# Performance work log

Measured on AMD Instinct MI355X. Metric: run time of the kernel, lower is better.

## Reference

```python
import jax, jax.numpy as jnp
import numpy as np

D = 1024          # label_size / in_features
V = 100000        # vocab size
SHORTLIST = 10000 # cutoffs[0]
# tail clusters: (proj_dim, cluster_size) per div_value=2 schedule
TAILS = [(512, 10000), (256, 20000), (128, 40000), (64, 20000)]


def setup_inputs() -> dict:
    key = jax.random.key(0)
    ks = jax.random.split(key, 11)
    s = jnp.float32(0.02)
    inp = {
        "feature": jax.random.normal(ks[0], (D,), jnp.float32),
        "targets": jax.random.randint(ks[1], (4096,), 0, V),
        "head_w": jax.random.normal(ks[2], (SHORTLIST + len(TAILS), D), jnp.float32) * s,
    }
    for i, (h, c) in enumerate(TAILS):
        inp[f"t{i}p"] = jax.random.normal(ks[3 + 2 * i], (h, D), jnp.float32) * s
        inp[f"t{i}w"] = jax.random.normal(ks[4 + 2 * i], (c, h), jnp.float32) * s
    return inp


def reference(feature, targets, head_w, t0p, t0w, t1p, t1w, t2p, t2w, t3p, t3w):
    # head logits: [SHORTLIST + n_clusters]
    head_lp = jax.nn.log_softmax(head_w @ feature)
    parts = [head_lp[:SHORTLIST]]
    tails = [(t0p, t0w), (t1p, t1w), (t2p, t2w), (t3p, t3w)]
    for i, (p, w) in enumerate(tails):
        # two-stage low-rank projection: [h] then cluster logits [c]
        cl_lp = jax.nn.log_softmax(w @ (p @ feature)) + head_lp[SHORTLIST + i]
        parts.append(cl_lp)
    logprob = jnp.concatenate(parts)  # [V] full-vocab log-probabilities
    return -jnp.mean(logprob[targets])
```

## Files before the change

### kernel.cpp

```cpp
#include <hip/hip_runtime.h>
#include <math.h>

#define NHEAD     10004
#define OFF_HEAD  0
#define OFF_H0    10004
#define OFF_H1    10516
#define OFF_H2    10772
#define OFF_H3    10900
#define OFF_C0    10964
#define OFF_C1    20964
#define OFF_C2    40964
#define OFF_C3    80964
#define OFF_P     100964
#define OFF_PH    100964
#define OFF_P0    101277
#define OFF_P1    101590
#define OFF_P2    101903
#define OFF_P3    102528
#define NPART     1877

__device__ __forceinline__ float wave_sum(float v) {
  v += __shfl_xor(v, 32, 64);
  v += __shfl_xor(v, 16, 64);
  v += __shfl_xor(v, 8, 64);
  v += __shfl_xor(v, 4, 64);
  v += __shfl_xor(v, 2, 64);
  v += __shfl_xor(v, 1, 64);
  return v;
}

__device__ __forceinline__ float dot4(float4 a, float4 c) {
  return a.x * c.x + a.y * c.y + a.z * c.z + a.w * c.w;
}

__global__ __launch_bounds__(256) void proj_kernel(
    const float* __restrict__ feat,
    const float* __restrict__ p0, const float* __restrict__ p1,
    const float* __restrict__ p2, const float* __restrict__ p3,
    float* __restrict__ ws) {
  __shared__ __align__(16) float sf[1024];
  ((float4*)sf)[threadIdx.x] = ((const float4*)feat)[threadIdx.x];
  __syncthreads();
  const float4* sf4 = (const float4*)sf;
  const int wave = threadIdx.x >> 6, lane = threadIdx.x & 63;
  const int pb = blockIdx.x;
#pragma unroll
  for (int k = 0; k < 4; ++k) {
    int row = NHEAD + pb * 16 + wave * 4 + k;
    const float* src;
    if (row < 10516)      src = p0 + (size_t)(row - 10004) * 1024;
    else if (row < 10772) src = p1 + (size_t)(row - 10516) * 1024;
    else if (row < 10900) src = p2 + (size_t)(row - 10772) * 1024;
    else                  src = p3 + (size_t)(row - 10900) * 1024;
    const float4* src4 = (const float4*)src;
    float acc = 0.f;
#pragma unroll
    for (int j = 0; j < 4; ++j) acc += dot4(src4[lane + j * 64], sf4[lane + j * 64]);
    acc = wave_sum(acc);
    if (lane == 0) ws[row] = acc;
  }
}

__global__ __launch_bounds__(256) void main_kernel(
    const float* __restrict__ feat, const float* __restrict__ head_w,
    const float* __restrict__ w0, const float* __restrict__ w1,
    const float* __restrict__ w2, const float* __restrict__ w3,
    float* __restrict__ ws) {
  __shared__ __align__(16) float sh[1024];
  __shared__ float wred[4];
  const int b = blockIdx.x;
  const int wave = threadIdx.x >> 6, lane = threadIdx.x & 63;
  float esum = 0.f;
  int poff, lb;

  if (b < 313) {
    lb = b; poff = OFF_PH;
    ((float4*)sh)[threadIdx.x] = ((const float4*)feat)[threadIdx.x];
    __syncthreads();
    const float4* sf4 = (const float4*)sh;
    const int row0 = lb * 32 + wave * 8;
#pragma unroll
    for (int k = 0; k < 8; ++k) {
      int row = row0 + k;
      int rc = min(row, NHEAD - 1);
      const float4* src4 = (const float4*)head_w + (size_t)rc * 256;
      float acc = 0.f;
#pragma unroll
      for (int j = 0; j < 4; ++j) acc += dot4(src4[lane + j * 64], sf4[lane + j * 64]);
      acc = wave_sum(acc);
      if (lane == 0 && row < NHEAD) { ws[OFF_HEAD + row] = acc; esum += expf(acc); }
    }
  } else if (b < 626) {
    lb = b - 313; poff = OFF_P0;
    if (threadIdx.x < 128) ((float4*)sh)[threadIdx.x] = ((const float4*)(ws + OFF_H0))[threadIdx.x];
    __syncthreads();
    const float4* sh4 = (const float4*)sh;
    const float4 cv0 = sh4[lane], cv1 = sh4[lane + 64];
    const int row0 = lb * 32 + wave * 8;
#pragma unroll
    for (int k = 0; k < 8; ++k) {
      int rc = min(row0 + k, 9999);
      const float4* wr4 = (const float4*)(w0 + (size_t)rc * 512);
      float acc = dot4(wr4[lane], cv0) + dot4(wr4[lane + 64], cv1);
      acc = wave_sum(acc);
      if (lane == 0 && row0 + k < 10000) { ws[OFF_C0 + row0 + k] = acc; esum += expf(acc); }
    }
  } else if (b < 939) {
    lb = b - 626; poff = OFF_P1;
    if (threadIdx.x < 64) ((float4*)sh)[threadIdx.x] = ((const float4*)(ws + OFF_H1))[threadIdx.x];
    __syncthreads();
    const float4 cv = ((const float4*)sh)[lane];
    const int row0 = lb * 64 + wave * 16;
#pragma unroll
    for (int k = 0; k < 16; ++k) {
      int rc = min(row0 + k, 19999);
      float acc = dot4(((const float4*)(w1 + (size_t)rc * 256))[lane], cv);
      acc = wave_sum(acc);
      if (lane == 0 && row0 + k < 20000) { ws[OFF_C1 + row0 + k] = acc; esum += expf(acc); }
    }
  } else if (b < 1564) {
    lb = b - 939; poff = OFF_P2;
    if (threadIdx.x < 32) ((float4*)sh)[threadIdx.x] = ((const float4*)(ws + OFF_H2))[threadIdx.x];
    __syncthreads();
    const float4 cv = ((const float4*)sh)[lane & 31];
    const int row0 = lb * 64 + wave * 16;
#pragma unroll
    for (int p = 0; p < 8; ++p) {
      int rbase = row0 + 2 * p;
      float acc = dot4(((const float4*)w2)[(size_t)rbase * 32 + lane], cv);
      acc += __shfl_xor(acc, 1, 64);
      acc += __shfl_xor(acc, 2, 64);
      acc += __shfl_xor(acc, 4, 64);
      acc += __shfl_xor(acc, 8, 64);
      acc += __shfl_xor(acc, 16, 64);
      if ((lane & 31) == 0) {
        int r = rbase + (lane >> 5);
        ws[OFF_C2 + r] = acc; esum += expf(acc);
      }
    }
  } else {
    lb = b - 1564; poff = OFF_P3;
    if (threadIdx.x < 16) ((float4*)sh)[threadIdx.x] = ((const float4*)(ws + OFF_H3))[threadIdx.x];
    __syncthreads();
    const float4 cv = ((const float4*)sh)[lane & 15];
    const int row0 = lb * 64 + wave * 16;
#pragma unroll
    for (int q = 0; q < 4; ++q) {
      int rb = row0 + 4 * q;
      int rbc = min(rb, 19996);
      float acc = dot4(((const float4*)w3)[(size_t)rbc * 16 + lane], cv);
      acc += __shfl_xor(acc, 1, 64);
      acc += __shfl_xor(acc, 2, 64);
      acc += __shfl_xor(acc, 4, 64);
      acc += __shfl_xor(acc, 8, 64);
      if ((lane & 15) == 0 && rb < 20000) {
        int r = rb + (lane >> 4);
        ws[OFF_C3 + r] = acc; esum += expf(acc);
      }
    }
  }
  esum = wave_sum(esum);
  if (lane == 0) wred[wave] = esum;
  __syncthreads();
  if (threadIdx.x == 0) ws[poff + lb] = wred[0] + wred[1] + wred[2] + wred[3];
}

__global__ __launch_bounds__(1024) void finalize_kernel(
    const int* __restrict__ targets, float* __restrict__ ws,
    float* __restrict__ out) {
  const int wv = threadIdx.x >> 6, lane = threadIdx.x & 63;
  float a0 = 0.f, a1 = 0.f, a2 = 0.f, a3 = 0.f, a4 = 0.f;
#pragma unroll
  for (int it = 0; it < 2; ++it) {
    int i = threadIdx.x + it * 1024;
    if (i < NPART) {
      float v = ws[OFF_P + i];
      if (i < 313)       a0 += v;
      else if (i < 626)  a1 += v;
      else if (i < 939)  a2 += v;
      else if (i < 1564) a3 += v;
      else               a4 += v;
    }
  }
  a0 = wave_sum(a0); a1 = wave_sum(a1); a2 = wave_sum(a2);
  a3 = wave_sum(a3); a4 = wave_sum(a4);
  __shared__ float r5[16][5];
  __shared__ float slse[5];
  if (lane == 0) { r5[wv][0] = a0; r5[wv][1] = a1; r5[wv][2] = a2; r5[wv][3] = a3; r5[wv][4] = a4; }
  __syncthreads();
  if (threadIdx.x < 5) {
    float s = 0.f;
#pragma unroll
    for (int w = 0; w < 16; ++w) s += r5[w][threadIdx.x];
    slse[threadIdx.x] = logf(s);
  }
  __syncthreads();
  const float lse0 = slse[0], lse1 = slse[1], lse2 = slse[2], lse3 = slse[3], lse4 = slse[4];
  const float g0 = ws[10000] - lse0, g1 = ws[10001] - lse0;
  const float g2 = ws[10002] - lse0, g3 = ws[10003] - lse0;
  float s = 0.f;
#pragma unroll
  for (int it = 0; it < 4; ++it) {
    int t = targets[threadIdx.x + it * 1024];
    float lp;
    if (t < 10000)      lp = ws[OFF_HEAD + t] - lse0;
    else if (t < 20000) lp = ws[OFF_C0 + t - 10000] - lse1 + g0;
    else if (t < 40000) lp = ws[OFF_C1 + t - 20000] - lse2 + g1;
    else if (t < 80000) lp = ws[OFF_C2 + t - 40000] - lse3 + g2;
    else                lp = ws[OFF_C3 + t - 80000] - lse4 + g3;
    s += lp;
  }
  s = wave_sum(s);
  if (lane == 0) r5[wv][0] = s;
  __syncthreads();
  if (threadIdx.x == 0) {
    float tot = 0.f;
#pragma unroll
    for (int w = 0; w < 16; ++w) tot += r5[w][0];
    out[0] = -tot * (1.f / 4096.f);
  }
}

extern "C" void kernel_launch(void* const* d_in, const int* in_sizes, int n_in,
                              void* d_out, int out_size, void* d_ws, size_t ws_size,
                              hipStream_t stream) {
  const float* feat    = (const float*)d_in[0];
  const int*   targets = (const int*)d_in[1];
  const float* head_w  = (const float*)d_in[2];
  const float* t0p = (const float*)d_in[3];
  const float* t0w = (const float*)d_in[4];
  const float* t1p = (const float*)d_in[5];
  const float* t1w = (const float*)d_in[6];
  const float* t2p = (const float*)d_in[7];
  const float* t2w = (const float*)d_in[8];
  const float* t3p = (const float*)d_in[9];
  const float* t3w = (const float*)d_in[10];
  float* ws  = (float*)d_ws;
  float* out = (float*)d_out;

  proj_kernel<<<60, 256, 0, stream>>>(feat, t0p, t1p, t2p, t3p, ws);
  main_kernel<<<1877, 256, 0, stream>>>(feat, head_w, t0w, t1w, t2w, t3w, ws);
  finalize_kernel<<<1, 1024, 0, stream>>>(targets, ws, out);
}
```

Measured before the change: 165.8 us.

## Restructure GEMV into per-wave persistent work units with batched loads

The projection kernel now gives one row per wave across 240 blocks, and loads are issued before the dot products. The main kernel becomes a grid-stride loop over per-wave units that cover every section. Each unit first issues 16 float4 loads, then computes and reduces, so more memory requests are in flight per wave. The block-level reduction and syncthreads are dropped in favour of per-wave partial sums. The finalize kernel prefetches target values with branchless addressing, which adds more partials to reduce and more register pressure per unit.

```diff
diff --git a/kernel.cpp b/kernel.cpp
--- a/kernel.cpp
+++ b/kernel.cpp
@@ -4,20 +4,19 @@
 #define NHEAD     10004
 #define OFF_HEAD  0
 #define OFF_H0    10004
-#define OFF_H1    10516
-#define OFF_H2    10772
-#define OFF_H3    10900
 #define OFF_C0    10964
 #define OFF_C1    20964
 #define OFF_C2    40964
 #define OFF_C3    80964
 #define OFF_P     100964
-#define OFF_PH    100964
-#define OFF_P0    101277
-#define OFF_P1    101590
-#define OFF_P2    101903
-#define OFF_P3    102528
-#define NPART     1877
+
+#define U_HEAD 2501
+#define B_C0   2501
+#define B_C1   3751
+#define B_C2   5001
+#define B_C3   6251
+#define NUNITS 6564
+#define NWAVES 3284
 
 __device__ __forceinline__ float wave_sum(float v) {
   v += __shfl_xor(v, 32, 64);
@@ -42,23 +41,133 @@
   ((float4*)sf)[threadIdx.x] = ((const float4*)feat)[threadIdx.x];
   __syncthreads();
   const float4* sf4 = (const float4*)sf;
-  const int wave = threadIdx.x >> 6, lane = threadIdx.x & 63;
-  const int pb = blockIdx.x;
-#pragma unroll
-  for (int k = 0; k < 4; ++k) {
-    int row = NHEAD + pb * 16 + wave * 4 + k;
-    const float* src;
-    if (row < 10516)      src = p0 + (size_t)(row - 10004) * 1024;
-    else if (row < 10772) src = p1 + (size_t)(row - 10516) * 1024;
-    else if (row < 10900) src = p2 + (size_t)(row - 10772) * 1024;
-    else                  src = p3 + (size_t)(row - 10900) * 1024;
-    const float4* src4 = (const float4*)src;
-    float acc = 0.f;
-#pragma unroll
-    for (int j = 0; j < 4; ++j) acc += dot4(src4[lane + j * 64], sf4[lane + j * 64]);
-    acc = wave_sum(acc);
-    if (lane == 0) ws[row] = acc;
-  }
+  const int lane = threadIdx.x & 63;
+  const int pr = blockIdx.x * 4 + (threadIdx.x >> 6);
+  const float* src;
+  if (pr < 512)      src = p0 + (size_t)pr * 1024;
+  else if (pr < 768) src = p1 + (size_t)(pr - 512) * 1024;
+  else if (pr < 896) src = p2 + (size_t)(pr - 768) * 1024;
+  else               src = p3 + (size_t)(pr - 896) * 1024;
+  const float4* src4 = (const float4*)src;
+  float4 ld[4];
+#pragma unroll
+  for (int j = 0; j < 4; ++j) ld[j] = src4[lane + j * 64];
+  float acc = 0.f;
+#pragma unroll
+  for (int j = 0; j < 4; ++j) acc += dot4(ld[j], sf4[lane + j * 64]);
+  acc = wave_sum(acc);
+  if (lane == 0) ws[NHEAD + pr] = acc;
+}
+
+__device__ __forceinline__ void process_unit(
+    int u, int lane, const float* sh,
+    const float* __restrict__ head_w, const float* __restrict__ w0,
+    const float* __restrict__ w1, const float* __restrict__ w2,
+    const float* __restrict__ w3, float* __restrict__ ws) {
+  float esum = 0.f;
+  if (u < B_C0) {
+    const float4* sf4 = (const float4*)sh;
+    const int r0 = u * 4;
+    float4 ld[16];
+#pragma unroll
+    for (int k = 0; k < 4; ++k) {
+      const float4* w4 = (const float4*)head_w + (size_t)(r0 + k) * 256;
+#pragma unroll
+      for (int j = 0; j < 4; ++j) ld[k * 4 + j] = w4[lane + j * 64];
+    }
+    float acc[4];
+#pragma unroll
+    for (int k = 0; k < 4; ++k) {
+      float a = 0.f;
+#pragma unroll
+      for (int j = 0; j < 4; ++j) a += dot4(ld[k * 4 + j], sf4[lane + j * 64]);
+      acc[k] = a;
+    }
+#pragma unroll
+    for (int k = 0; k < 4; ++k) {
+      float a = wave_sum(acc[k]);
+      if (lane == 0) { ws[OFF_HEAD + r0 + k] = a; esum += expf(a); }
+    }
+  } else if (u < B_C1) {
+    const float4* h4 = (const float4*)(sh + 1024);
+    const float4 cv0 = h4[lane], cv1 = h4[lane + 64];
+    const int r0 = (u - B_C0) * 8;
+    float4 ld[16];
+#pragma unroll
+    for (int k = 0; k < 8; ++k) {
+      const float4* w4 = (const float4*)w0 + (size_t)(r0 + k) * 128;
+      ld[k * 2] = w4[lane]; ld[k * 2 + 1] = w4[lane + 64];
+    }
+    float acc[8];
+#pragma unroll
+    for (int k = 0; k < 8; ++k)
+      acc[k] = dot4(ld[k * 2], cv0) + dot4(ld[k * 2 + 1], cv1);
+#pragma unroll
+    for (int k = 0; k < 8; ++k) {
+      float a = wave_sum(acc[k]);
+      if (lane == 0) { ws[OFF_C0 + r0 + k] = a; esum += expf(a); }
+    }
+  } else if (u < B_C2) {
+    const float4 cv = ((const float4*)(sh + 1536))[lane];
+    const int r0 = (u - B_C1) * 16;
+    float4 ld[16];
+#pragma unroll
+    for (int k = 0; k < 16; ++k)
+      ld[k] = ((const float4*)w1)[(size_t)(r0 + k) * 64 + lane];
+    float acc[16];
+#pragma unroll
+    for (int k = 0; k < 16; ++k) acc[k] = dot4(ld[k], cv);
+#pragma unroll
+    for (int k = 0; k < 16; ++k) {
+      float a = wave_sum(acc[k]);
+      if (lane == 0) { ws[OFF_C1 + r0 + k] = a; esum += expf(a); }
+    }
+  } else if (u < B_C3) {
+    const float4 cv = ((const float4*)(sh + 1792))[lane & 31];
+    const int r0 = (u - B_C2) * 32;
+    float4 ld[16];
+#pragma unroll
+    for (int p = 0; p < 16; ++p)
+      ld[p] = ((const float4*)w2)[(size_t)(r0 + 2 * p) * 32 + lane];
+#pragma unroll
+    for (int p = 0; p < 16; ++p) {
+      float a = dot4(ld[p], cv);
+      a += __shfl_xor(a, 1, 64);
+      a += __shfl_xor(a, 2, 64);
+      a += __shfl_xor(a, 4, 64);
+      a += __shfl_xor(a, 8, 64);
+      a += __shfl_xor(a, 16, 64);
+      if ((lane & 31) == 0) {
+        int r = r0 + 2 * p + (lane >> 5);
+        ws[OFF_C2 + r] = a; esum += expf(a);
+      }
+    }
+  } else {
+    const float4 cv = ((const float4*)(sh + 1920))[lane & 15];
+    const int r0 = (u - B_C3) * 64;
+    float4 ld[16];
+#pragma unroll
+    for (int p = 0; p < 16; ++p) {
+      int rb = r0 + 4 * p;
+      int rbc = min(rb, 19996);
+      ld[p] = ((const float4*)w3)[(size_t)rbc * 16 + lane];
+    }
+#pragma unroll
+    for (int p = 0; p < 16; ++p) {
+      int rb = r0 + 4 * p;
+      float a = dot4(ld[p], cv);
+      a += __shfl_xor(a, 1, 64);
+      a += __shfl_xor(a, 2, 64);
+      a += __shfl_xor(a, 4, 64);
+      a += __shfl_xor(a, 8, 64);
+      if ((lane & 15) == 0 && rb < 20000) {
+        int r = rb + (lane >> 4);
+        ws[OFF_C3 + r] = a; esum += expf(a);
+      }
+    }
+  }
+  esum = wave_sum(esum);
+  if (lane == 0) ws[OFF_P + u] = esum;
 }
 
 __global__ __launch_bounds__(256) void main_kernel(
@@ -66,119 +175,41 @@
     const float* __restrict__ w0, const float* __restrict__ w1,
     const float* __restrict__ w2, const float* __restrict__ w3,
     float* __restrict__ ws) {
-  __shared__ __align__(16) float sh[1024];
-  __shared__ float wred[4];
-  const int b = blockIdx.x;
-  const int wave = threadIdx.x >> 6, lane = threadIdx.x & 63;
-  float esum = 0.f;
-  int poff, lb;
-
-  if (b < 313) {
-    lb = b; poff = OFF_PH;
-    ((float4*)sh)[threadIdx.x] = ((const float4*)feat)[threadIdx.x];
-    __syncthreads();
-    const float4* sf4 = (const float4*)sh;
-    const int row0 = lb * 32 + wave * 8;
-#pragma unroll
-    for (int k = 0; k < 8; ++k) {
-      int row = row0 + k;
-      int rc = min(row, NHEAD - 1);
-      const float4* src4 = (const float4*)head_w + (size_t)rc * 256;
-      float acc = 0.f;
-#pragma unroll
-      for (int j = 0; j < 4; ++j) acc += dot4(src4[lane + j * 64], sf4[lane + j * 64]);
-      acc = wave_sum(acc);
-      if (lane == 0 && row < NHEAD) { ws[OFF_HEAD + row] = acc; esum += expf(acc); }
-    }
-  } else if (b < 626) {
-    lb = b - 313; poff = OFF_P0;
-    if (threadIdx.x < 128) ((float4*)sh)[threadIdx.x] = ((const float4*)(ws + OFF_H0))[threadIdx.x];
-    __syncthreads();
-    const float4* sh4 = (const float4*)sh;
-    const float4 cv0 = sh4[lane], cv1 = sh4[lane + 64];
-    const int row0 = lb * 32 + wave * 8;
-#pragma unroll
-    for (int k = 0; k < 8; ++k) {
-      int rc = min(row0 + k, 9999);
-      const float4* wr4 = (const float4*)(w0 + (size_t)rc * 512);
-      float acc = dot4(wr4[lane], cv0) + dot4(wr4[lane + 64], cv1);
-      acc = wave_sum(acc);
-      if (lane == 0 && row0 + k < 10000) { ws[OFF_C0 + row0 + k] = acc; esum += expf(acc); }
-    }
-  } else if (b < 939) {
-    lb = b - 626; poff = OFF_P1;
-    if (threadIdx.x < 64) ((float4*)sh)[threadIdx.x] = ((const float4*)(ws + OFF_H1))[threadIdx.x];
-    __syncthreads();
-    const float4 cv = ((const float4*)sh)[lane];
-    const int row0 = lb * 64 + wave * 16;
-#pragma unroll
-    for (int k = 0; k < 16; ++k) {
-      int rc = min(row0 + k, 19999);
-      float acc = dot4(((const float4*)(w1 + (size_t)rc * 256))[lane], cv);
-      acc = wave_sum(acc);
-      if (lane == 0 && row0 + k < 20000) { ws[OFF_C1 + row0 + k] = acc; esum += expf(acc); }
-    }
-  } else if (b < 1564) {
-    lb = b - 939; poff = OFF_P2;
-    if (threadIdx.x < 32) ((float4*)sh)[threadIdx.x] = ((const float4*)(ws + OFF_H2))[threadIdx.x];
-    __syncthreads();
-    const float4 cv = ((const float4*)sh)[lane & 31];
-    const int row0 = lb * 64 + wave * 16;
-#pragma unroll
-    for (int p = 0; p < 8; ++p) {
-      int rbase = row0 + 2 * p;
-      float acc = dot4(((const float4*)w2)[(size_t)rbase * 32 + lane], cv);
-      acc += __shfl_xor(acc, 1, 64);
-      acc += __shfl_xor(acc, 2, 64);
-      acc += __shfl_xor(acc, 4, 64);
-      acc += __shfl_xor(acc, 8, 64);
-      acc += __shfl_xor(acc, 16, 64);
-      if ((lane & 31) == 0) {
-        int r = rbase + (lane >> 5);
-        ws[OFF_C2 + r] = acc; esum += expf(acc);
-      }
-    }
-  } else {
-    lb = b - 1564; poff = OFF_P3;
-    if (threadIdx.x < 16) ((float4*)sh)[threadIdx.x] = ((const float4*)(ws + OFF_H3))[threadIdx.x];
-    __syncthreads();
-    const float4 cv = ((const float4*)sh)[lane & 15];
-    const int row0 = lb * 64 + wave * 16;
-#pragma unroll
-    for (int q = 0; q < 4; ++q) {
-      int rb = row0 + 4 * q;
-      int rbc = min(rb, 19996);
-      float acc = dot4(((const float4*)w3)[(size_t)rbc * 16 + lane], cv);
-      acc += __shfl_xor(acc, 1, 64);
-      acc += __shfl_xor(acc, 2, 64);
-      acc += __shfl_xor(acc, 4, 64);
-      acc += __shfl_xor(acc, 8, 64);
-      if ((lane & 15) == 0 && rb < 20000) {
-        int r = rb + (lane >> 4);
-        ws[OFF_C3 + r] = acc; esum += expf(acc);
-      }
-    }
-  }
-  esum = wave_sum(esum);
-  if (lane == 0) wred[wave] = esum;
-  __syncthreads();
-  if (threadIdx.x == 0) ws[poff + lb] = wred[0] + wred[1] + wred[2] + wred[3];
+  __shared__ __align__(16) float sh[1984];
+  const int t = threadIdx.x;
+  ((float4*)sh)[t] = ((const float4*)feat)[t];
+  if (t < 240) ((float4*)(sh + 1024))[t] = ((const float4*)(ws + OFF_H0))[t];
+  __syncthreads();
+  const int lane = t & 63;
+  const int wid = blockIdx.x * 4 + (t >> 6);
+#pragma unroll 1
+  for (int u = wid; u < NUNITS; u += NWAVES)
+    process_unit(u, lane, sh, head_w, w0, w1, w2, w3, ws);
 }
 
 __global__ __launch_bounds__(1024) void finalize_kernel(
     const int* __restrict__ targets, float* __restrict__ ws,
     float* __restrict__ out) {
-  const int wv = threadIdx.x >> 6, lane = threadIdx.x & 63;
+  const int tid = threadIdx.x;
+  const int wv = tid >> 6, lane = tid & 63;
+  float tv[4]; int sg[4];
+#pragma unroll
+  for (int it = 0; it < 4; ++it) {
+    int tgt = targets[tid + it * 1024];
+    int addr = tgt + ((tgt >= 10000) ? 964 : 0);
+    tv[it] = ws[addr];
+    sg[it] = (tgt >= 10000) + (tgt >= 20000) + (tgt >= 40000) + (tgt >= 80000);
+  }
   float a0 = 0.f, a1 = 0.f, a2 = 0.f, a3 = 0.f, a4 = 0.f;
 #pragma unroll
-  for (int it = 0; it < 2; ++it) {
-    int i = threadIdx.x + it * 1024;
-    if (i < NPART) {
+  for (int it = 0; it < 7; ++it) {
+    int i = tid + it * 1024;
+    if (i < NUNITS) {
       float v = ws[OFF_P + i];
-      if (i < 313)       a0 += v;
-      else if (i < 626)  a1 += v;
-      else if (i < 939)  a2 += v;
-      else if (i < 1564) a3 += v;
+      if (i < B_C0)      a0 += v;
+      else if (i < B_C1) a1 += v;
+      else if (i < B_C2) a2 += v;
+      else if (i < B_C3) a3 += v;
       else               a4 += v;
     }
   }
@@ -188,11 +219,11 @@
   __shared__ float slse[5];
   if (lane == 0) { r5[wv][0] = a0; r5[wv][1] = a1; r5[wv][2] = a2; r5[wv][3] = a3; r5[wv][4] = a4; }
   __syncthreads();
-  if (threadIdx.x < 5) {
+  if (tid < 5) {
     float s = 0.f;
 #pragma unroll
-    for (int w = 0; w < 16; ++w) s += r5[w][threadIdx.x];
-    slse[threadIdx.x] = logf(s);
+    for (int w = 0; w < 16; ++w) s += r5[w][tid];
+    slse[tid] = logf(s);
   }
   __syncthreads();
   const float lse0 = slse[0], lse1 = slse[1], lse2 = slse[2], lse3 = slse[3], lse4 = slse[4];
@@ -201,19 +232,15 @@
   float s = 0.f;
 #pragma unroll
   for (int it = 0; it < 4; ++it) {
-    int t = targets[threadIdx.x + it * 1024];
-    float lp;
-    if (t < 10000)      lp = ws[OFF_HEAD + t] - lse0;
-    else if (t < 20000) lp = ws[OFF_C0 + t - 10000] - lse1 + g0;
-    else if (t < 40000) lp = ws[OFF_C1 + t - 20000] - lse2 + g1;
-    else if (t < 80000) lp = ws[OFF_C2 + t - 40000] - lse3 + g2;
-    else                lp = ws[OFF_C3 + t - 80000] - lse4 + g3;
-    s += lp;
+    int e = sg[it];
+    float lseS = (e == 0) ? lse0 : (e == 1) ? lse1 : (e == 2) ? lse2 : (e == 3) ? lse3 : lse4;
+    float gS   = (e == 0) ? 0.f  : (e == 1) ? g0   : (e == 2) ? g1   : (e == 3) ? g2   : g3;
+    s += tv[it] - lseS + gS;
   }
   s = wave_sum(s);
   if (lane == 0) r5[wv][0] = s;
   __syncthreads();
-  if (threadIdx.x == 0) {
+  if (tid == 0) {
     float tot = 0.f;
 #pragma unroll
     for (int w = 0; w < 16; ++w) tot += r5[w][0];
@@ -238,7 +265,7 @@
   float* ws  = (float*)d_ws;
   float* out = (float*)d_out;
 
-  proj_kernel<<<60, 256, 0, stream>>>(feat, t0p, t1p, t2p, t3p, ws);
-  main_kernel<<<1877, 256, 0, stream>>>(feat, head_w, t0w, t1w, t2w, t3w, ws);
+  proj_kernel<<<240, 256, 0, stream>>>(feat, t0p, t1p, t2p, t3p, ws);
+  main_kernel<<<821, 256, 0, stream>>>(feat, head_w, t0w, t1w, t2w, t3w, ws);
   finalize_kernel<<<1, 1024, 0, stream>>>(targets, ws, out);
 }
```

After: 166.3 us. Within noise of the previous version (+0.3%).
